# Kernel optimization log

Hardware: AMD Instinct MI355X
Metric: run time of the kernel (lower is better)

Reference implementation:

```python
import jax, jax.numpy as jnp
import numpy as np
from jax import lax

B, N, C, NP, NS, H, L = 2, 16384, 256, 2048, 32, 4, 2
DFF = 2 * C
RADIUS = 1.0
EPS = 1e-5


def setup_inputs() -> dict:
    key = jax.random.key(0)
    ks = jax.random.split(key, 12)
    s = 0.02
    f32 = jnp.float32
    return {
        "xyz": jax.random.normal(ks[0], (B, N, 3), f32),
        "features": jax.random.normal(ks[1], (B, C, N), f32),
        # positional encoding: Conv1x1(3->C/2)+BN(eval)+ReLU, Conv1x1(C/2->C)
        "pe1_w": jax.random.normal(ks[2], (C // 2, 3), f32) * s,
        "pe1_b": jnp.zeros((C // 2,), f32),
        "bn_g": jnp.ones((C // 2,), f32),
        "bn_b": jnp.zeros((C // 2,), f32),
        "bn_m": jnp.zeros((C // 2,), f32),
        "bn_v": jnp.ones((C // 2,), f32),
        "pe2_w": jax.random.normal(ks[3], (C, C // 2), f32) * s,
        "pe2_b": jnp.zeros((C,), f32),
        # L pre-norm transformer encoder layers (stacked on leading dim)
        "ipw": jax.random.normal(ks[4], (L, 3 * C, C), f32) * s,
        "ipb": jnp.zeros((L, 3 * C), f32),
        "opw": jax.random.normal(ks[5], (L, C, C), f32) * s,
        "opb": jnp.zeros((L, C), f32),
        "ln1s": jnp.ones((L, C), f32), "ln1b": jnp.zeros((L, C), f32),
        "ln2s": jnp.ones((L, C), f32), "ln2b": jnp.zeros((L, C), f32),
        "fc1w": jax.random.normal(ks[6], (L, DFF, C), f32) * s,
        "fc1b": jnp.zeros((L, DFF), f32),
        "fc2w": jax.random.normal(ks[7], (L, C, DFF), f32) * s,
        "fc2b": jnp.zeros((L, C), f32),
    }


def _fps(xyz, npoint):
    # D-FPS starting from point 0 (pointnet2 convention). xyz: [B,N,3]
    b, n, _ = xyz.shape

    def step(carry, _):
        dists, far = carry
        centroid = jnp.take_along_axis(xyz, far[:, None, None], axis=1)  # [B,1,3]
        d = jnp.sum((xyz - centroid) ** 2, -1)
        dists = jnp.minimum(dists, d)
        return (dists, jnp.argmax(dists, -1).astype(jnp.int32)), far

    init = (jnp.full((b, n), 1e10, jnp.float32), jnp.zeros((b,), jnp.int32))
    _, idx = lax.scan(step, init, None, length=npoint)
    return idx.T  # [B, npoint]


def _ball_query(xyz, new_xyz, radius, ns):
    # first <=ns points within radius, padded with the first hit. [B,NP,NS]
    n = xyz.shape[1]
    d2 = jnp.sum((new_xyz[:, :, None, :] - xyz[:, None, :, :]) ** 2, -1)  # [B,NP,N]
    scores = jnp.where(d2 < radius * radius, jnp.arange(n, dtype=jnp.int32), n)
    svals = jnp.sort(scores, axis=-1)[..., :ns]
    order = jnp.argsort(scores, axis=-1)[..., :ns].astype(jnp.int32)
    valid = svals < n
    return jnp.where(valid, order, order[..., :1])


def _ln(x, s, b):
    m = jnp.mean(x, -1, keepdims=True)
    v = jnp.var(x, -1, keepdims=True)
    return (x - m) * lax.rsqrt(v + EPS) * s + b


def _mha(x, w, bias, ow, ob):
    # x: [S, Bn, D] (seq-first, like nn.MultiheadAttention)
    S, Bn, D = x.shape
    hd = D // H
    qkv = x @ w.T + bias
    q, k, v = jnp.split(qkv, 3, -1)
    rs = lambda t: t.reshape(S, Bn, H, hd).transpose(1, 2, 0, 3)  # [Bn,H,S,hd]
    q, k, v = rs(q), rs(k), rs(v)
    att = jax.nn.softmax(jnp.einsum('bhqd,bhkd->bhqk', q, k) * (1.0 / np.sqrt(hd)), -1)
    o = jnp.einsum('bhqk,bhkd->bhqd', att, v).transpose(2, 0, 1, 3).reshape(S, Bn, D)
    return o @ ow.T + ob


def reference(xyz, features, pe1_w, pe1_b, bn_g, bn_b, bn_m, bn_v, pe2_w, pe2_b,
              ipw, ipb, opw, opb, ln1s, ln1b, ln2s, ln2b, fc1w, fc1b, fc2w, fc2b):
    # --- sample + group ---
    fps_idx = _fps(lax.stop_gradient(xyz), NP)                       # [B,NP]
    new_xyz = jnp.take_along_axis(xyz, fps_idx[:, :, None], axis=1)  # [B,NP,3]
    idx = _ball_query(lax.stop_gradient(xyz), lax.stop_gradient(new_xyz), RADIUS, NS)
    g_xyz = jax.vmap(lambda p, i: p[i])(xyz, idx) - new_xyz[:, :, None, :]  # [B,NP,NS,3]
    g_xyz = g_xyz.transpose(0, 3, 1, 2)                              # [B,3,NP,NS]
    g_feat = jax.vmap(lambda f, i: f[:, i])(features, idx)           # [B,C,NP,NS]
    # --- positional encoding (conv1x1 + BN(eval) + ReLU, conv1x1) ---
    h = jnp.einsum('oc,bcps->bops', pe1_w, g_xyz) + pe1_b[None, :, None, None]
    h = (h - bn_m[None, :, None, None]) * lax.rsqrt(bn_v + EPS)[None, :, None, None]
    h = jax.nn.relu(h * bn_g[None, :, None, None] + bn_b[None, :, None, None])
    pe = jnp.einsum('oc,bcps->bops', pe2_w, h) + pe2_b[None, :, None, None]
    x = g_feat + pe                                                  # [B,C,NP,NS]
    # --- local transformer over each neighborhood (seq len = NS) ---
    x = x.transpose(0, 2, 1, 3).reshape(B * NP, C, NS).transpose(2, 0, 1)  # [NS,B*NP,C]
    for l in range(L):
        x = _ln(x, ln1s[l], ln1b[l])
        x = x + _mha(x, ipw[l], ipb[l], opw[l], opb[l])
        x = _ln(x, ln2s[l], ln2b[l])
        x = x + jax.nn.relu(x @ fc1w[l].T + fc1b[l]) @ fc2w[l].T + fc2b[l]
    tf = x.transpose(1, 2, 0).reshape(B, NP, C, NS).transpose(0, 2, 1, 3)  # [B,C,NP,NS]
    Lf = NP * NS

    def scat(feat_b, tf_b, idx_b):
        idx_f = idx_b.reshape(-1)          # [Lf]
        ff = tf_b.reshape(C, -1)           # [C,Lf]
        pos = jnp.arange(Lf, dtype=jnp.int32)
        first = jax.ops.segment_min(pos, idx_f, num_segments=N)  # [N], maxint if absent
        valid = first < Lf
        safe = jnp.where(valid, first, 0)
        return jnp.where(valid[None, :], ff[:, safe], feat_b)    # [C,N]

    out = jax.vmap(scat)(features, tf, idx)  # [B,C,N]
    return out.transpose(0, 2, 1)            # [B,N,C]
```

## Files before the change

kernel.cpp:

```cpp
#include <hip/hip_runtime.h>

#define NB 2
#define NN 16384
#define NC 256
#define NPp 2048
#define NSs 32
#define NH 4
#define HDh 64
#define NL 2
#define NDFF 512
#define LFv (NPp*NSs)
#define LNEPS 1e-5f
#define NBLK 256
#define NTHR 512

typedef short s16x8 __attribute__((ext_vector_type(8)));
typedef float f32x4 __attribute__((ext_vector_type(4)));
typedef float f32x2 __attribute__((ext_vector_type(2)));
typedef unsigned short u16;
typedef unsigned long long u64;

struct CtlBlock { int prog[2]; int ctr1; int ctr2; int bar; };

__device__ __forceinline__ u16 f2bf(float f){
  unsigned u = __float_as_uint(f);
  u += 0x7fffu + ((u>>16)&1u);
  return (u16)(u>>16);
}

__device__ __forceinline__ f32x4 mfma16(s16x8 a, s16x8 b, f32x4 c){
  return __builtin_amdgcn_mfma_f32_16x16x32_bf16(a, b, c, 0, 0, 0);
}

__device__ __forceinline__ f32x2 pk_add(f32x2 a, f32x2 b){
  f32x2 d; asm("v_pk_add_f32 %0, %1, %2" : "=v"(d) : "v"(a), "v"(b)); return d;
}
__device__ __forceinline__ f32x2 pk_mul(f32x2 a, f32x2 b){
  f32x2 d; asm("v_pk_mul_f32 %0, %1, %2" : "=v"(d) : "v"(a), "v"(b)); return d;
}

#define DPP_FMAX(v, ctrl) do { \
  int _iv = __float_as_int(v); \
  int _sh = __builtin_amdgcn_update_dpp(_iv, _iv, (ctrl), 0xF, 0xF, false); \
  (v) = fmaxf((v), __int_as_float(_sh)); \
} while(0)

#define DPP_IMIN(v, ctrl) do { \
  int _sh = __builtin_amdgcn_update_dpp((v), (v), (ctrl), 0xF, 0xF, false); \
  (v) = (_sh < (v)) ? _sh : (v); \
} while(0)

struct SMem {
  u64  masks[256];
  u64  wvkey[2][8];
  float wvc[2][8][4];
  int  idxbuf[8];
  float xs[32][260];
  u16  xn[32][264];
  u16  qb[32][776];
  u16  pb[NH][32][40];
  int  idx_sh[32];
  float gx_sh[32][3];
  int  misc[16];
  int  win[32];
};

__global__ void k_prep(const float* __restrict__ ipw, const float* __restrict__ opw,
                       const float* __restrict__ fc1w, const float* __restrict__ fc2w,
                       const float* __restrict__ pe2w,
                       const float* __restrict__ bng, const float* __restrict__ bnb,
                       const float* __restrict__ bnm, const float* __restrict__ bnv,
                       u16* ipwb, u16* opwb, u16* fc1wb, u16* fc2wb, u16* pe2wb,
                       float* bnsc, float* bnsh, int* first, CtlBlock* ctl){
  const int i0 = blockIdx.x*blockDim.x + threadIdx.x;
  const int stride = gridDim.x*blockDim.x;
  for (int i=i0; i<NL*768*NC; i+=stride) ipwb[i] = f2bf(ipw[i]);
  for (int i=i0; i<NL*NC*NC; i+=stride)  opwb[i] = f2bf(opw[i]);
  for (int i=i0; i<NL*NDFF*NC; i+=stride) fc1wb[i] = f2bf(fc1w[i]);
  for (int i=i0; i<NL*NC*NDFF; i+=stride) fc2wb[i] = f2bf(fc2w[i]);
  for (int i=i0; i<NC*128; i+=stride)    pe2wb[i] = f2bf(pe2w[i]);
  for (int i=i0; i<NB*NN; i+=stride)     first[i] = LFv;
  for (int i=i0; i<128; i+=stride){
    float sc = bng[i]*rsqrtf(bnv[i]+LNEPS);
    bnsc[i] = sc; bnsh[i] = bnb[i] - bnm[i]*sc;
  }
  if (i0 == 0){
    ctl->prog[0] = -1; ctl->prog[1] = -1;
    ctl->ctr1 = 0; ctl->ctr2 = 0; ctl->bar = 0;
  }
}

__global__ __launch_bounds__(256) void k_featT(const float* __restrict__ feat,
                                               float* __restrict__ featT){
  __shared__ float T[32][33];
  const int b = blockIdx.y;
  const int n0 = blockIdx.x*32;
  const int t = threadIdx.x;
  const int tn = t & 31, tc = t >> 5;
  for (int cb=0; cb<NC; cb+=32){
    #pragma unroll
    for (int i=0;i<32;i+=8)
      T[tc+i][tn] = feat[((size_t)b*NC + cb+tc+i)*NN + n0+tn];
    __syncthreads();
    #pragma unroll
    for (int i=0;i<32;i+=8)
      featT[((size_t)b*NN + n0+tc+i)*NC + cb+tn] = T[tn][tc+i];
    __syncthreads();
  }
}

#define SELC(S) case S: scx = px2[(S)>>1][(S)&1]; scy = py2[(S)>>1][(S)&1]; scz = pz2[(S)>>1][(S)&1]; break;

__device__ void fps_run(int b, const float* __restrict__ xyz, int* __restrict__ fps_idx,
                        CtlBlock* ctl, SMem& sm){
#pragma clang fp contract(off)
  const int t = threadIdx.x;
  const int lane = t & 63, wid = t >> 6;
  const float* xb = xyz + (size_t)b*NN*3;
  f32x2 px2[16], py2[16], pz2[16], dd2[16];
  #pragma unroll
  for (int m=0;m<16;m++){
    int i0 = t + (2*m)*NTHR, i1 = t + (2*m+1)*NTHR;
    px2[m] = f32x2{xb[i0*3],   xb[i1*3]};
    py2[m] = f32x2{xb[i0*3+1], xb[i1*3+1]};
    pz2[m] = f32x2{xb[i0*3+2], xb[i1*3+2]};
    dd2[m] = f32x2{1e10f, 1e10f};
  }
  float ncx, ncy, ncz;
  {
    float wx = xb[0], wy = xb[1], wz = xb[2];
    ncx=-wx; ncy=-wy; ncz=-wz;
    if (t==0){
      fps_idx[b*NPp] = 0;
      __hip_atomic_store(&ctl->prog[b], 0, __ATOMIC_RELEASE, __HIP_MEMORY_SCOPE_AGENT);
    }
  }
  __syncthreads();
  for (int step=1; step<NPp; ++step){
    const f32x2 ncx2={ncx,ncx}, ncy2={ncy,ncy}, ncz2={ncz,ncz};
    #pragma unroll
    for (int m=0;m<16;m++){
      f32x2 dx = pk_add(px2[m], ncx2);
      f32x2 dy = pk_add(py2[m], ncy2);
      f32x2 dz = pk_add(pz2[m], ncz2);
      f32x2 s  = pk_add(pk_add(pk_mul(dx,dx), pk_mul(dy,dy)), pk_mul(dz,dz));
      f32x2 d  = dd2[m];
      d.x = fminf(d.x, s.x);
      d.y = fminf(d.y, s.y);
      dd2[m] = d;
    }
    float h8[8];
    #pragma unroll
    for (int q=0;q<8;q++)
      h8[q] = fmaxf(fmaxf(dd2[2*q].x, dd2[2*q].y), fmaxf(dd2[2*q+1].x, dd2[2*q+1].y));
    float M = fmaxf(fmaxf(fmaxf(h8[0],h8[1]),fmaxf(h8[2],h8[3])),
                    fmaxf(fmaxf(h8[4],h8[5]),fmaxf(h8[6],h8[7])));
    DPP_FMAX(M, 0x111); DPP_FMAX(M, 0x112); DPP_FMAX(M, 0x114); DPP_FMAX(M, 0x118);
    DPP_FMAX(M, 0x142); DPP_FMAX(M, 0x143);
    const int Mi = __builtin_amdgcn_readlane(__float_as_int(M), 63);
    const float Ms = __int_as_float(Mi);
    int li = 0x7fffffff;
    #pragma unroll
    for (int m=15;m>=0;m--){
      if (dd2[m].y == Ms) li = t + (2*m+1)*NTHR;
      if (dd2[m].x == Ms) li = t + (2*m)*NTHR;
    }
    DPP_IMIN(li, 0x111); DPP_IMIN(li, 0x112); DPP_IMIN(li, 0x114); DPP_IMIN(li, 0x118);
    DPP_IMIN(li, 0x142); DPP_IMIN(li, 0x143);
    const int liw = __builtin_amdgcn_readlane(li, 63);
    const int sb = step & 1;
    if (lane==0)
      sm.wvkey[sb][wid] = ((u64)(unsigned)Mi << 32) | (unsigned)(0x7fffffff - liw);
    {
      const int slot = liw >> 9;
      float scx=0.f, scy=0.f, scz=0.f;
      switch(slot){
        SELC(0) SELC(1) SELC(2) SELC(3) SELC(4) SELC(5) SELC(6) SELC(7)
        SELC(8) SELC(9) SELC(10) SELC(11) SELC(12) SELC(13) SELC(14) SELC(15)
        SELC(16) SELC(17) SELC(18) SELC(19) SELC(20) SELC(21) SELC(22) SELC(23)
        SELC(24) SELC(25) SELC(26) SELC(27) SELC(28) SELC(29) SELC(30) SELC(31)
        default: break;
      }
      if (t == (liw & (NTHR-1))){
        sm.wvc[sb][wid][0]=scx; sm.wvc[sb][wid][1]=scy; sm.wvc[sb][wid][2]=scz;
      }
    }
    __syncthreads();
    u64 bk = sm.wvkey[sb][0];
    float bx=sm.wvc[sb][0][0], by=sm.wvc[sb][0][1], bz=sm.wvc[sb][0][2];
    #pragma unroll
    for (int w=1;w<8;w++){
      u64 k2 = sm.wvkey[sb][w];
      if (k2 > bk){ bk=k2; bx=sm.wvc[sb][w][0]; by=sm.wvc[sb][w][1]; bz=sm.wvc[sb][w][2]; }
    }
    ncx=-bx; ncy=-by; ncz=-bz;
    if (t==0){
      int widx = 0x7fffffff - (int)(unsigned)(bk & 0xffffffffu);
      sm.idxbuf[step & 7] = widx;
      if ((step & 7) == 7){
        int s0 = step - 7;
        #pragma unroll
        for (int j=0;j<8;j++){
          int s = s0 + j;
          if (s > 0) fps_idx[b*NPp + s] = sm.idxbuf[s & 7];
        }
        __hip_atomic_store(&ctl->prog[b], step, __ATOMIC_RELEASE, __HIP_MEMORY_SCOPE_AGENT);
      }
    }
  }
}

__device__ void seq_ballq(const float* __restrict__ xb, float cx, float cy, float cz,
                          SMem& sm, int t, int lane, int wid){
#pragma clang fp contract(off)
  for (int it=0; it<32; ++it){
    int cid = wid*32 + it;
    int i = cid*64 + lane;
    float dx=xb[i*3]-cx, dy=xb[i*3+1]-cy, dz=xb[i*3+2]-cz;
    float d2=(dx*dx+dy*dy)+dz*dz;
    u64 m = __ballot(d2 < 1.0f);
    if (lane==0) sm.masks[cid] = m;
  }
  __syncthreads();
  if (wid==0){
    u64 mk[4]; int cnt=0;
    #pragma unroll
    for (int j=0;j<4;j++){ mk[j]=sm.masks[lane*4+j]; cnt += __popcll(mk[j]); }
    int inc = cnt;
    #pragma unroll
    for (int ofs=1; ofs<64; ofs<<=1){
      int v = __shfl_up(inc, ofs);
      if (lane >= ofs) inc += v;
    }
    int r = inc - cnt;
    int tot = __shfl(inc, 63);
    #pragma unroll
    for (int j=0;j<4;j++){
      u64 msk = mk[j];
      int base = (lane*4+j)*64;
      while (msk && r < NSs){
        int bpos = __ffsll(msk)-1;
        sm.idx_sh[r] = base + bpos;
        msk &= msk-1;
        ++r;
      }
      if (r >= NSs) break;
    }
    int cc = tot < NSs ? tot : NSs;
    int pv = (tot > 0) ? sm.idx_sh[0] : 0;
    if (lane < NSs && lane >= cc) sm.idx_sh[lane] = pv;
  }
  __syncthreads();
}

__device__ __forceinline__ void ln_block512(SMem& sm, const float* __restrict__ s_,
                                            const float* __restrict__ b_, int t){
  const int s = t >> 4, j = t & 15;
  float v[16];
  float sum = 0.f;
  #pragma unroll
  for (int k=0;k<16;k++){ v[k]=sm.xs[s][j*16+k]; sum += v[k]; }
  #pragma unroll
  for (int m=1;m<16;m<<=1) sum += __shfl_xor(sum, m);
  const float mean = sum * (1.f/256.f);
  float vs = 0.f;
  #pragma unroll
  for (int k=0;k<16;k++){ float d=v[k]-mean; vs += d*d; }
  #pragma unroll
  for (int m=1;m<16;m<<=1) vs += __shfl_xor(vs, m);
  const float rstd = rsqrtf(vs*(1.f/256.f) + LNEPS);
  #pragma unroll
  for (int k=0;k<16;k++){
    int c = j*16+k;
    float y = (v[k]-mean)*rstd*s_[c] + b_[c];
    sm.xs[s][c] = y;
    sm.xn[s][c] = f2bf(y);
  }
}

__device__ void seq_pe_tf(SMem& sm, int b, float ccx, float ccy, float ccz,
    const float* __restrict__ xyz, const float* __restrict__ features,
    const float* __restrict__ featT, int useT,
    const float* __restrict__ pe1w, const float* __restrict__ pe1b,
    const float* __restrict__ bnsc, const float* __restrict__ bnsh,
    const u16* __restrict__ pe2wb, const float* __restrict__ pe2b,
    const u16* __restrict__ ipwb, const float* __restrict__ ipb,
    const u16* __restrict__ opwb, const float* __restrict__ opb,
    const float* __restrict__ ln1s, const float* __restrict__ ln1b,
    const float* __restrict__ ln2s, const float* __restrict__ ln2b,
    const u16* __restrict__ fc1wb, const float* __restrict__ fc1b,
    const u16* __restrict__ fc2wb, const float* __restrict__ fc2b){
  const int t = threadIdx.x, lane = t & 63, wid = t >> 6;
  const int c15 = lane & 15, g4 = lane >> 4;

  if (t < 96){
    int s = t/3, d = t%3;
    float cd = (d==0) ? ccx : ((d==1) ? ccy : ccz);
    sm.gx_sh[s][d] = xyz[((size_t)b*NN + sm.idx_sh[s])*3 + d] - cd;
  }
  if (useT){
    for (int e=t; e<32*NC; e+=NTHR){
      int s=e>>8, c=e&255;
      sm.xs[s][c] = featT[((size_t)b*NN + sm.idx_sh[s])*NC + c];
    }
  } else {
    for (int e=t; e<32*NC; e+=NTHR){
      int s=e>>8, c=e&255;
      sm.xs[s][c] = features[((size_t)b*NC + c)*NN + sm.idx_sh[s]];
    }
  }
  __syncthreads();
  for (int i=t; i<32*128; i+=NTHR){
    int s = i >> 7, o = i & 127;
    float h = pe1w[o*3]*sm.gx_sh[s][0] + pe1w[o*3+1]*sm.gx_sh[s][1] + pe1w[o*3+2]*sm.gx_sh[s][2] + pe1b[o];
    h = h*bnsc[o] + bnsh[o];
    sm.xn[s][o] = f2bf(h > 0.f ? h : 0.f);
  }
  __syncthreads();
  for (int tt=wid; tt<32; tt+=8){
    int m0 = (tt & 1)*16, n0 = (tt >> 1)*16;
    f32x4 acc = {0.f,0.f,0.f,0.f};
    #pragma unroll
    for (int kk=0; kk<4; kk++){
      s16x8 a = *(const s16x8*)&sm.xn[m0+c15][kk*32 + g4*8];
      s16x8 bb = *(const s16x8*)&pe2wb[(size_t)(n0+c15)*128 + kk*32 + g4*8];
      acc = mfma16(a, bb, acc);
    }
    int col = n0 + c15;
    float bias = pe2b[col];
    #pragma unroll
    for (int r=0;r<4;r++) sm.xs[m0 + g4*4 + r][col] += acc[r] + bias;
  }
  __syncthreads();

  for (int l=0; l<NL; ++l){
    ln_block512(sm, ln1s + l*NC, ln1b + l*NC, t);
    __syncthreads();
    const u16* Wq = ipwb + (size_t)l*768*NC;
    const float* bq = ipb + l*768;
    for (int tt=wid; tt<96; tt+=8){
      int m0 = (tt & 1)*16, n0 = (tt >> 1)*16;
      f32x4 acc = {0.f,0.f,0.f,0.f};
      #pragma unroll
      for (int kk=0;kk<8;kk++){
        s16x8 a = *(const s16x8*)&sm.xn[m0+c15][kk*32 + g4*8];
        s16x8 bb = *(const s16x8*)&Wq[(size_t)(n0+c15)*NC + kk*32 + g4*8];
        acc = mfma16(a, bb, acc);
      }
      int col = n0 + c15;
      float bias = bq[col];
      #pragma unroll
      for (int r=0;r<4;r++) sm.qb[m0 + g4*4 + r][col] = f2bf(acc[r] + bias);
    }
    __syncthreads();
    {
      const int h = wid & 3;
      const int mt = wid >> 2;
      f32x4 lac[2];
      #pragma unroll
      for (int nt=0;nt<2;nt++){
        f32x4 acc = {0.f,0.f,0.f,0.f};
        #pragma unroll
        for (int kk=0;kk<2;kk++){
          s16x8 a = *(const s16x8*)&sm.qb[mt*16+c15][h*HDh + kk*32 + g4*8];
          s16x8 bb = *(const s16x8*)&sm.qb[nt*16+c15][256 + h*HDh + kk*32 + g4*8];
          acc = mfma16(a, bb, acc);
        }
        lac[nt] = acc;
      }
      #pragma unroll
      for (int r=0;r<4;r++){
        float v0 = lac[0][r]*0.125f, v1 = lac[1][r]*0.125f;
        float mx = fmaxf(v0, v1);
        #pragma unroll
        for (int m=1;m<16;m<<=1) mx = fmaxf(mx, __shfl_xor(mx, m));
        float e0 = expf(v0-mx), e1 = expf(v1-mx);
        float smm = e0 + e1;
        #pragma unroll
        for (int m=1;m<16;m<<=1) smm += __shfl_xor(smm, m);
        float inv = 1.f/smm;
        int row = mt*16 + g4*4 + r;
        sm.pb[h][row][c15]    = f2bf(e0*inv);
        sm.pb[h][row][16+c15] = f2bf(e1*inv);
      }
      f32x4 oac[4];
      #pragma unroll
      for (int nt=0;nt<4;nt++){
        s16x8 bb;
        #pragma unroll
        for (int e=0;e<8;e++) bb[e] = (short)sm.qb[g4*8+e][512 + h*HDh + nt*16 + c15];
        f32x4 acc = {0.f,0.f,0.f,0.f};
        s16x8 a = *(const s16x8*)&sm.pb[h][mt*16+c15][g4*8];
        oac[nt] = mfma16(a, bb, acc);
      }
      __syncthreads();
      #pragma unroll
      for (int nt=0;nt<4;nt++)
        #pragma unroll
        for (int r=0;r<4;r++)
          sm.xn[mt*16 + g4*4 + r][h*HDh + nt*16 + c15] = f2bf(oac[nt][r]);
    }
    __syncthreads();
    const u16* Wo = opwb + (size_t)l*NC*NC;
    const float* bo = opb + l*NC;
    for (int tt=wid; tt<32; tt+=8){
      int m0 = (tt & 1)*16, n0 = (tt >> 1)*16;
      f32x4 acc = {0.f,0.f,0.f,0.f};
      #pragma unroll
      for (int kk=0;kk<8;kk++){
        s16x8 a = *(const s16x8*)&sm.xn[m0+c15][kk*32 + g4*8];
        s16x8 bb = *(const s16x8*)&Wo[(size_t)(n0+c15)*NC + kk*32 + g4*8];
        acc = mfma16(a, bb, acc);
      }
      int col = n0 + c15;
      float bias = bo[col];
      #pragma unroll
      for (int r=0;r<4;r++) sm.xs[m0 + g4*4 + r][col] += acc[r] + bias;
    }
    __syncthreads();
    ln_block512(sm, ln2s + l*NC, ln2b + l*NC, t);
    __syncthreads();
    const u16* W1 = fc1wb + (size_t)l*NDFF*NC;
    for (int tt=wid; tt<64; tt+=8){
      int m0 = (tt & 1)*16, n0 = (tt >> 1)*16;
      f32x4 acc = {0.f,0.f,0.f,0.f};
      #pragma unroll
      for (int kk=0;kk<8;kk++){
        s16x8 a = *(const s16x8*)&sm.xn[m0+c15][kk*32 + g4*8];
        s16x8 bb = *(const s16x8*)&W1[(size_t)(n0+c15)*NC + kk*32 + g4*8];
        acc = mfma16(a, bb, acc);
      }
      int col = n0 + c15;
      float bias = fc1b[l*NDFF + col];
      #pragma unroll
      for (int r=0;r<4;r++){
        float v = acc[r] + bias;
        sm.qb[m0 + g4*4 + r][col] = f2bf(v > 0.f ? v : 0.f);
      }
    }
    __syncthreads();
    const u16* W2 = fc2wb + (size_t)l*NC*NDFF;
    for (int tt=wid; tt<32; tt+=8){
      int m0 = (tt & 1)*16, n0 = (tt >> 1)*16;
      f32x4 acc = {0.f,0.f,0.f,0.f};
      #pragma unroll
      for (int kk=0;kk<16;kk++){
        s16x8 a = *(const s16x8*)&sm.qb[m0+c15][kk*32 + g4*8];
        s16x8 bb = *(const s16x8*)&W2[(size_t)(n0+c15)*NDFF + kk*32 + g4*8];
        acc = mfma16(a, bb, acc);
      }
      int col = n0 + c15;
      float bias = fc2b[l*NC + col];
      #pragma unroll
      for (int r=0;r<4;r++) sm.xs[m0 + g4*4 + r][col] += acc[r] + bias;
    }
    __syncthreads();
  }
}

__global__ __launch_bounds__(NTHR,1) void k_mega(
    const float* __restrict__ xyz, const float* __restrict__ features,
    const float* __restrict__ featT, int useT, u16* __restrict__ tfb, int spec,
    int* __restrict__ fps_idx, int* __restrict__ first, CtlBlock* ctl,
    const float* __restrict__ pe1w, const float* __restrict__ pe1b,
    const float* __restrict__ bnsc, const float* __restrict__ bnsh,
    const u16* __restrict__ pe2wb, const float* __restrict__ pe2b,
    const u16* __restrict__ ipwb, const float* __restrict__ ipb,
    const u16* __restrict__ opwb, const float* __restrict__ opb,
    const float* __restrict__ ln1s, const float* __restrict__ ln1b,
    const float* __restrict__ ln2s, const float* __restrict__ ln2b,
    const u16* __restrict__ fc1wb, const float* __restrict__ fc1b,
    const u16* __restrict__ fc2wb, const float* __restrict__ fc2b,
    float* __restrict__ out){
  __shared__ SMem sm;
  const int t = threadIdx.x, lane = t & 63, wid = t >> 6;

  if (blockIdx.x < NB){
    fps_run(blockIdx.x, xyz, fps_idx, ctl, sm);
  } else {
    for (;;){
      if (t==0) sm.misc[1] = atomicAdd(&ctl->ctr1, 1);
      __syncthreads();
      int p = sm.misc[1];
      if (p >= NB*NPp) break;
      int b = p >> 11, pp = p & (NPp-1);
      if (t==0){
        while (__hip_atomic_load(&ctl->prog[b], __ATOMIC_RELAXED, __HIP_MEMORY_SCOPE_AGENT) < pp)
          __builtin_amdgcn_s_sleep(2);
        __builtin_amdgcn_fence(__ATOMIC_ACQUIRE, "agent");
        sm.misc[4] = fps_idx[p];
      }
      __syncthreads();
      int ci = sm.misc[4];
      float cx = xyz[((size_t)b*NN + ci)*3];
      float cy = xyz[((size_t)b*NN + ci)*3+1];
      float cz = xyz[((size_t)b*NN + ci)*3+2];
      seq_ballq(xyz + (size_t)b*NN*3, cx, cy, cz, sm, t, lane, wid);
      if (t < NSs) atomicMin(&first[b*NN + sm.idx_sh[t]], pp*NSs + t);
      if (spec){
        seq_pe_tf(sm, b, cx, cy, cz, xyz, features, featT, useT,
                  pe1w, pe1b, bnsc, bnsh, pe2wb, pe2b, ipwb, ipb, opwb, opb,
                  ln1s, ln1b, ln2s, ln2b, fc1wb, fc1b, fc2wb, fc2b);
        for (int e=t; e<NSs*NC; e+=NTHR)
          tfb[(size_t)p*NSs*NC + e] = f2bf(sm.xs[e>>8][e&255]);
      }
      __syncthreads();
    }
  }
  if (spec) return;

  __syncthreads();
  if (t==0){
    __builtin_amdgcn_fence(__ATOMIC_RELEASE, "agent");
    __hip_atomic_fetch_add(&ctl->bar, 1, __ATOMIC_RELAXED, __HIP_MEMORY_SCOPE_AGENT);
    while (__hip_atomic_load(&ctl->bar, __ATOMIC_RELAXED, __HIP_MEMORY_SCOPE_AGENT) < NBLK)
      __builtin_amdgcn_s_sleep(8);
    __builtin_amdgcn_fence(__ATOMIC_ACQUIRE, "agent");
  }
  __syncthreads();
  for (;;){
    if (t==0) sm.misc[1] = atomicAdd(&ctl->ctr2, 1);
    __syncthreads();
    int p = sm.misc[1];
    if (p >= NB*NPp) break;
    int b = p >> 11, pp = p & (NPp-1);
    int ci = fps_idx[p];
    float cx = xyz[((size_t)b*NN + ci)*3];
    float cy = xyz[((size_t)b*NN + ci)*3+1];
    float cz = xyz[((size_t)b*NN + ci)*3+2];
    seq_ballq(xyz + (size_t)b*NN*3, cx, cy, cz, sm, t, lane, wid);
    if (t==0) sm.misc[2] = 0;
    __syncthreads();
    if (t < NSs){
      int pos = pp*NSs + t;
      int f = __hip_atomic_load(&first[b*NN + sm.idx_sh[t]], __ATOMIC_RELAXED, __HIP_MEMORY_SCOPE_AGENT);
      int w = (f == pos) ? 1 : 0;
      sm.win[t] = w;
      if (w) atomicOr(&sm.misc[2], 1);
    }
    __syncthreads();
    if (!sm.misc[2]) continue;
    seq_pe_tf(sm, b, cx, cy, cz, xyz, features, featT, useT,
              pe1w, pe1b, bnsc, bnsh, pe2wb, pe2b, ipwb, ipb, opwb, opb,
              ln1s, ln1b, ln2s, ln2b, fc1wb, fc1b, fc2wb, fc2b);
    for (int e=t; e<NSs*NC; e+=NTHR){
      int s = e >> 8, c = e & 255;
      if (sm.win[s]) out[((size_t)b*NN + sm.idx_sh[s])*NC + c] = sm.xs[s][c];
    }
    __syncthreads();
  }
}

__global__ __launch_bounds__(256) void k_commit(const u16* __restrict__ tfb,
                                                const int* __restrict__ first,
                                                const float* __restrict__ featT,
                                                const float* __restrict__ feat,
                                                int useT, float* __restrict__ out){
  const int t = threadIdx.x;
  const int row0 = blockIdx.x*16;
  for (int r=0;r<16;++r){
    int row = row0 + r;
    int b = row >> 14;
    int f = first[row];
    float v;
    if (f != LFv){
      unsigned u = tfb[((size_t)b*NPp*NSs + f)*NC + t];
      v = __int_as_float((int)(u << 16));
    } else if (useT){
      v = featT[(size_t)row*NC + t];
    } else {
      int n = row & (NN-1);
      v = feat[((size_t)b*NC + t)*NN + n];
    }
    out[(size_t)row*NC + t] = v;
  }
}

__global__ __launch_bounds__(256) void k_outfill_T(const float* __restrict__ featT,
                                                   const int* __restrict__ first,
                                                   float* __restrict__ out){
  const int t = threadIdx.x;
  for (int rr=0; rr<8; ++rr){
    int row = blockIdx.x*8 + rr;
    if (first[row] == LFv)
      out[(size_t)row*NC + t] = featT[(size_t)row*NC + t];
  }
}

__global__ __launch_bounds__(256) void k_outfill_noT(const float* __restrict__ feat,
                                                     const int* __restrict__ first,
                                                     float* __restrict__ out){
  __shared__ float T[32][33];
  const int b = blockIdx.y;
  const int n0 = blockIdx.x*32;
  const int t = threadIdx.x;
  const int tn = t & 31, tc = t >> 5;
  for (int cb=0; cb<NC; cb+=32){
    #pragma unroll
    for (int i=0;i<32;i+=8)
      T[tc+i][tn] = feat[((size_t)b*NC + cb+tc+i)*NN + n0+tn];
    __syncthreads();
    #pragma unroll
    for (int i=0;i<32;i+=8){
      int n = n0 + tc + i;
      if (first[b*NN+n] == LFv)
        out[((size_t)b*NN + n)*NC + cb+tn] = T[tn][tc+i];
    }
    __syncthreads();
  }
}

extern "C" void kernel_launch(void* const* d_in, const int* in_sizes, int n_in,
                              void* d_out, int out_size, void* d_ws, size_t ws_size,
                              hipStream_t stream){
  const float* xyz   = (const float*)d_in[0];
  const float* feat  = (const float*)d_in[1];
  const float* pe1w  = (const float*)d_in[2];
  const float* pe1b  = (const float*)d_in[3];
  const float* bng   = (const float*)d_in[4];
  const float* bnb   = (const float*)d_in[5];
  const float* bnm   = (const float*)d_in[6];
  const float* bnv   = (const float*)d_in[7];
  const float* pe2w  = (const float*)d_in[8];
  const float* pe2b  = (const float*)d_in[9];
  const float* ipw   = (const float*)d_in[10];
  const float* ipb   = (const float*)d_in[11];
  const float* opw   = (const float*)d_in[12];
  const float* opb   = (const float*)d_in[13];
  const float* ln1s  = (const float*)d_in[14];
  const float* ln1b  = (const float*)d_in[15];
  const float* ln2s  = (const float*)d_in[16];
  const float* ln2b  = (const float*)d_in[17];
  const float* fc1w  = (const float*)d_in[18];
  const float* fc1b  = (const float*)d_in[19];
  const float* fc2w  = (const float*)d_in[20];
  const float* fc2b  = (const float*)d_in[21];
  float* out = (float*)d_out;

  char* ws = (char*)d_ws;
  size_t off = 0;
  auto alloc = [&](size_t bytes)->void*{
    void* p = ws + off;
    off = (off + bytes + 255) & ~(size_t)255;
    return p;
  };
  int*   fps_idx = (int*)  alloc((size_t)NB*NPp*4);
  int*   first   = (int*)  alloc((size_t)NB*NN*4);
  CtlBlock* ctl  = (CtlBlock*)alloc(sizeof(CtlBlock));
  float* bnsc    = (float*)alloc(128*4);
  float* bnsh    = (float*)alloc(128*4);
  u16*   ipwb    = (u16*)  alloc((size_t)NL*768*NC*2);
  u16*   opwb    = (u16*)  alloc((size_t)NL*NC*NC*2);
  u16*   fc1wb   = (u16*)  alloc((size_t)NL*NDFF*NC*2);
  u16*   fc2wb   = (u16*)  alloc((size_t)NL*NC*NDFF*2);
  u16*   pe2wb   = (u16*)  alloc((size_t)NC*128*2);
  int useT = (off + (size_t)NB*NN*NC*4 <= ws_size) ? 1 : 0;
  float* featT = (float*)(useT ? alloc((size_t)NB*NN*NC*4) : (void*)ws);
  int spec = (off + (size_t)NB*NPp*NSs*NC*2 <= ws_size) ? 1 : 0;
  u16* tfb = (u16*)(spec ? alloc((size_t)NB*NPp*NSs*NC*2) : (void*)ws);

  k_prep<<<512, 256, 0, stream>>>(ipw, opw, fc1w, fc2w, pe2w, bng, bnb, bnm, bnv,
                                  ipwb, opwb, fc1wb, fc2wb, pe2wb, bnsc, bnsh, first, ctl);
  if (useT)
    k_featT<<<dim3(NN/32, NB), 256, 0, stream>>>(feat, featT);

  const float* featT_c = featT;
  void* kargs[] = {
    (void*)&xyz, (void*)&feat, (void*)&featT_c, (void*)&useT, (void*)&tfb, (void*)&spec,
    (void*)&fps_idx, (void*)&first, (void*)&ctl,
    (void*)&pe1w, (void*)&pe1b, (void*)&bnsc, (void*)&bnsh,
    (void*)&pe2wb, (void*)&pe2b, (void*)&ipwb, (void*)&ipb,
    (void*)&opwb, (void*)&opb, (void*)&ln1s, (void*)&ln1b,
    (void*)&ln2s, (void*)&ln2b, (void*)&fc1wb, (void*)&fc1b,
    (void*)&fc2wb, (void*)&fc2b, (void*)&out };
  hipLaunchCooperativeKernel((void*)k_mega, dim3(NBLK), dim3(NTHR), kargs, 0, stream);

  if (spec){
    k_commit<<<(NB*NN)/16, 256, 0, stream>>>(tfb, first, featT, feat, useT, out);
  } else if (useT){
    k_outfill_T<<<(NB*NN)/8, 256, 0, stream>>>(featT, first, out);
  } else {
    k_outfill_noT<<<dim3(NN/32, NB), 256, 0, stream>>>(feat, first, out);
  }
  (void)in_sizes; (void)n_in; (void)out_size;
}
```

Baseline: 5.295 ms.

## Double block size to 1024 threads and publish FPS centroid coordinates directly

Raises the persistent kernel's block size from 512 to 1024 threads (16 waves), so each FPS block holds fewer points per thread and the transformer GEMM loops spread over more waves. The FPS argmax index search now uses per-wave ballots and a shuffle reduction instead of DPP min chains and a serial scan. Consumers read centroid xyz published as packed 64-bit words rather than an index followed by a dependent xyz gather. Acquire/release ordering is replaced with relaxed atomics plus explicit waitcnt, and progress is published one step later. This adds register pressure, idles half the waves in attention, and relies on hand-written memory ordering for correctness.

```diff
diff --git a/kernel.cpp b/kernel.cpp
--- a/kernel.cpp
+++ b/kernel.cpp
@@ -12,7 +12,8 @@
 #define LFv (NPp*NSs)
 #define LNEPS 1e-5f
 #define NBLK 256
-#define NTHR 512
+#define NTHR 1024
+#define NW 16
 
 typedef short s16x8 __attribute__((ext_vector_type(8)));
 typedef float f32x4 __attribute__((ext_vector_type(4)));
@@ -45,16 +46,11 @@
   (v) = fmaxf((v), __int_as_float(_sh)); \
 } while(0)
 
-#define DPP_IMIN(v, ctrl) do { \
-  int _sh = __builtin_amdgcn_update_dpp((v), (v), (ctrl), 0xF, 0xF, false); \
-  (v) = (_sh < (v)) ? _sh : (v); \
-} while(0)
-
 struct SMem {
   u64  masks[256];
-  u64  wvkey[2][8];
-  float wvc[2][8][4];
-  int  idxbuf[8];
+  u64  wvkey[2][NW];
+  float wvc[2][NW][4];
+  float cxbuf[8][4];
   float xs[32][260];
   u16  xn[32][264];
   u16  qb[32][776];
@@ -111,15 +107,16 @@
 
 #define SELC(S) case S: scx = px2[(S)>>1][(S)&1]; scy = py2[(S)>>1][(S)&1]; scz = pz2[(S)>>1][(S)&1]; break;
 
-__device__ void fps_run(int b, const float* __restrict__ xyz, int* __restrict__ fps_idx,
+__device__ void fps_run(int b, const float* __restrict__ xyz, u64* __restrict__ cx2,
                         CtlBlock* ctl, SMem& sm){
 #pragma clang fp contract(off)
   const int t = threadIdx.x;
   const int lane = t & 63, wid = t >> 6;
+  const int wbase = wid*64;
   const float* xb = xyz + (size_t)b*NN*3;
-  f32x2 px2[16], py2[16], pz2[16], dd2[16];
+  f32x2 px2[8], py2[8], pz2[8], dd2[8];
   #pragma unroll
-  for (int m=0;m<16;m++){
+  for (int m=0;m<8;m++){
     int i0 = t + (2*m)*NTHR, i1 = t + (2*m+1)*NTHR;
     px2[m] = f32x2{xb[i0*3],   xb[i1*3]};
     py2[m] = f32x2{xb[i0*3+1], xb[i1*3+1]};
@@ -131,15 +128,21 @@
     float wx = xb[0], wy = xb[1], wz = xb[2];
     ncx=-wx; ncy=-wy; ncz=-wz;
     if (t==0){
-      fps_idx[b*NPp] = 0;
-      __hip_atomic_store(&ctl->prog[b], 0, __ATOMIC_RELEASE, __HIP_MEMORY_SCOPE_AGENT);
+      sm.cxbuf[0][0]=wx; sm.cxbuf[0][1]=wy; sm.cxbuf[0][2]=wz;
+      u64 lo = ((u64)__float_as_uint(wy) << 32) | __float_as_uint(wx);
+      u64 hi = (u64)__float_as_uint(wz);
+      __hip_atomic_store(&cx2[(size_t)(b*NPp)*2],   lo, __ATOMIC_RELAXED, __HIP_MEMORY_SCOPE_AGENT);
+      __hip_atomic_store(&cx2[(size_t)(b*NPp)*2+1], hi, __ATOMIC_RELAXED, __HIP_MEMORY_SCOPE_AGENT);
+      asm volatile("s_waitcnt vmcnt(0)" ::: "memory");
+      __hip_atomic_store(&ctl->prog[b], 0, __ATOMIC_RELAXED, __HIP_MEMORY_SCOPE_AGENT);
     }
   }
   __syncthreads();
   for (int step=1; step<NPp; ++step){
     const f32x2 ncx2={ncx,ncx}, ncy2={ncy,ncy}, ncz2={ncz,ncz};
-    #pragma unroll
-    for (int m=0;m<16;m++){
+    float bestv = -1.f;
+    #pragma unroll
+    for (int m=0;m<8;m++){
       f32x2 dx = pk_add(px2[m], ncx2);
       f32x2 dy = pk_add(py2[m], ncy2);
       f32x2 dz = pk_add(pz2[m], ncz2);
@@ -148,73 +151,82 @@
       d.x = fminf(d.x, s.x);
       d.y = fminf(d.y, s.y);
       dd2[m] = d;
-    }
-    float h8[8];
-    #pragma unroll
-    for (int q=0;q<8;q++)
-      h8[q] = fmaxf(fmaxf(dd2[2*q].x, dd2[2*q].y), fmaxf(dd2[2*q+1].x, dd2[2*q+1].y));
-    float M = fmaxf(fmaxf(fmaxf(h8[0],h8[1]),fmaxf(h8[2],h8[3])),
-                    fmaxf(fmaxf(h8[4],h8[5]),fmaxf(h8[6],h8[7])));
+      bestv = fmaxf(fmaxf(bestv, d.x), d.y);
+    }
+    float M = bestv;
     DPP_FMAX(M, 0x111); DPP_FMAX(M, 0x112); DPP_FMAX(M, 0x114); DPP_FMAX(M, 0x118);
     DPP_FMAX(M, 0x142); DPP_FMAX(M, 0x143);
     const int Mi = __builtin_amdgcn_readlane(__float_as_int(M), 63);
     const float Ms = __int_as_float(Mi);
-    int li = 0x7fffffff;
-    #pragma unroll
-    for (int m=15;m>=0;m--){
-      if (dd2[m].y == Ms) li = t + (2*m+1)*NTHR;
-      if (dd2[m].x == Ms) li = t + (2*m)*NTHR;
-    }
-    DPP_IMIN(li, 0x111); DPP_IMIN(li, 0x112); DPP_IMIN(li, 0x114); DPP_IMIN(li, 0x118);
-    DPP_IMIN(li, 0x142); DPP_IMIN(li, 0x143);
-    const int liw = __builtin_amdgcn_readlane(li, 63);
+    u64 bs[16];
+    #pragma unroll
+    for (int m=0;m<8;m++){
+      bs[2*m]   = __ballot(dd2[m].x == Ms);
+      bs[2*m+1] = __ballot(dd2[m].y == Ms);
+    }
+    int li = 0;
+    #pragma unroll
+    for (int s=15;s>=0;s--)
+      if (bs[s]) li = wbase + s*NTHR + (__ffsll(bs[s])-1);
     const int sb = step & 1;
     if (lane==0)
-      sm.wvkey[sb][wid] = ((u64)(unsigned)Mi << 32) | (unsigned)(0x7fffffff - liw);
+      sm.wvkey[sb][wid] = ((u64)(unsigned)Mi << 32) | (unsigned)(0x7fffffff - li);
     {
-      const int slot = liw >> 9;
+      const int slot = li >> 10;
       float scx=0.f, scy=0.f, scz=0.f;
       switch(slot){
         SELC(0) SELC(1) SELC(2) SELC(3) SELC(4) SELC(5) SELC(6) SELC(7)
         SELC(8) SELC(9) SELC(10) SELC(11) SELC(12) SELC(13) SELC(14) SELC(15)
-        SELC(16) SELC(17) SELC(18) SELC(19) SELC(20) SELC(21) SELC(22) SELC(23)
-        SELC(24) SELC(25) SELC(26) SELC(27) SELC(28) SELC(29) SELC(30) SELC(31)
         default: break;
       }
-      if (t == (liw & (NTHR-1))){
+      if (t == (li & (NTHR-1))){
         sm.wvc[sb][wid][0]=scx; sm.wvc[sb][wid][1]=scy; sm.wvc[sb][wid][2]=scz;
       }
     }
     __syncthreads();
-    u64 bk = sm.wvkey[sb][0];
-    float bx=sm.wvc[sb][0][0], by=sm.wvc[sb][0][1], bz=sm.wvc[sb][0][2];
-    #pragma unroll
-    for (int w=1;w<8;w++){
-      u64 k2 = sm.wvkey[sb][w];
-      if (k2 > bk){ bk=k2; bx=sm.wvc[sb][w][0]; by=sm.wvc[sb][w][1]; bz=sm.wvc[sb][w][2]; }
-    }
+    u64 v = sm.wvkey[sb][lane & 15];
+    #pragma unroll
+    for (int m=1;m<16;m<<=1){
+      u64 o = __shfl_xor(v, m);
+      if (o > v) v = o;
+    }
+    const int widx = 0x7fffffff - (int)(unsigned)(v & 0xffffffffull);
+    const int wv = (widx & (NTHR-1)) >> 6;
+    const float bx = sm.wvc[sb][wv][0];
+    const float by = sm.wvc[sb][wv][1];
+    const float bz = sm.wvc[sb][wv][2];
     ncx=-bx; ncy=-by; ncz=-bz;
     if (t==0){
-      int widx = 0x7fffffff - (int)(unsigned)(bk & 0xffffffffu);
-      sm.idxbuf[step & 7] = widx;
+      sm.cxbuf[step & 7][0]=bx; sm.cxbuf[step & 7][1]=by; sm.cxbuf[step & 7][2]=bz;
       if ((step & 7) == 7){
         int s0 = step - 7;
         #pragma unroll
         for (int j=0;j<8;j++){
-          int s = s0 + j;
-          if (s > 0) fps_idx[b*NPp + s] = sm.idxbuf[s & 7];
+          float fx=sm.cxbuf[j][0], fy=sm.cxbuf[j][1], fz=sm.cxbuf[j][2];
+          u64 lo = ((u64)__float_as_uint(fy) << 32) | __float_as_uint(fx);
+          u64 hi = (u64)__float_as_uint(fz);
+          size_t pb2 = (size_t)(b*NPp + s0 + j)*2;
+          __hip_atomic_store(&cx2[pb2],   lo, __ATOMIC_RELAXED, __HIP_MEMORY_SCOPE_AGENT);
+          __hip_atomic_store(&cx2[pb2+1], hi, __ATOMIC_RELAXED, __HIP_MEMORY_SCOPE_AGENT);
         }
-        __hip_atomic_store(&ctl->prog[b], step, __ATOMIC_RELEASE, __HIP_MEMORY_SCOPE_AGENT);
-      }
-    }
+      }
+      if ((step & 7) == 0){
+        asm volatile("s_waitcnt vmcnt(0)" ::: "memory");
+        __hip_atomic_store(&ctl->prog[b], step-1, __ATOMIC_RELAXED, __HIP_MEMORY_SCOPE_AGENT);
+      }
+    }
+  }
+  if (t==0){
+    asm volatile("s_waitcnt vmcnt(0)" ::: "memory");
+    __hip_atomic_store(&ctl->prog[b], NPp, __ATOMIC_RELAXED, __HIP_MEMORY_SCOPE_AGENT);
   }
 }
 
 __device__ void seq_ballq(const float* __restrict__ xb, float cx, float cy, float cz,
                           SMem& sm, int t, int lane, int wid){
 #pragma clang fp contract(off)
-  for (int it=0; it<32; ++it){
-    int cid = wid*32 + it;
+  for (int it=0; it<16; ++it){
+    int cid = wid*16 + it;
     int i = cid*64 + lane;
     float dx=xb[i*3]-cx, dy=xb[i*3+1]-cy, dz=xb[i*3+2]-cz;
     float d2=(dx*dx+dy*dy)+dz*dz;
@@ -253,25 +265,25 @@
   __syncthreads();
 }
 
-__device__ __forceinline__ void ln_block512(SMem& sm, const float* __restrict__ s_,
-                                            const float* __restrict__ b_, int t){
-  const int s = t >> 4, j = t & 15;
-  float v[16];
+__device__ __forceinline__ void ln_block1024(SMem& sm, const float* __restrict__ s_,
+                                             const float* __restrict__ b_, int t){
+  const int s = t >> 5, j = t & 31;
+  float v[8];
   float sum = 0.f;
   #pragma unroll
-  for (int k=0;k<16;k++){ v[k]=sm.xs[s][j*16+k]; sum += v[k]; }
+  for (int k=0;k<8;k++){ v[k]=sm.xs[s][j*8+k]; sum += v[k]; }
   #pragma unroll
-  for (int m=1;m<16;m<<=1) sum += __shfl_xor(sum, m);
+  for (int m=1;m<32;m<<=1) sum += __shfl_xor(sum, m);
   const float mean = sum * (1.f/256.f);
   float vs = 0.f;
   #pragma unroll
-  for (int k=0;k<16;k++){ float d=v[k]-mean; vs += d*d; }
+  for (int k=0;k<8;k++){ float d=v[k]-mean; vs += d*d; }
   #pragma unroll
-  for (int m=1;m<16;m<<=1) vs += __shfl_xor(vs, m);
+  for (int m=1;m<32;m<<=1) vs += __shfl_xor(vs, m);
   const float rstd = rsqrtf(vs*(1.f/256.f) + LNEPS);
   #pragma unroll
-  for (int k=0;k<16;k++){
-    int c = j*16+k;
+  for (int k=0;k<8;k++){
+    int c = j*8+k;
     float y = (v[k]-mean)*rstd*s_[c] + b_[c];
     sm.xs[s][c] = y;
     sm.xn[s][c] = f2bf(y);
@@ -317,7 +329,7 @@
     sm.xn[s][o] = f2bf(h > 0.f ? h : 0.f);
   }
   __syncthreads();
-  for (int tt=wid; tt<32; tt+=8){
+  for (int tt=wid; tt<32; tt+=NW){
     int m0 = (tt & 1)*16, n0 = (tt >> 1)*16;
     f32x4 acc = {0.f,0.f,0.f,0.f};
     #pragma unroll
@@ -334,11 +346,11 @@
   __syncthreads();
 
   for (int l=0; l<NL; ++l){
-    ln_block512(sm, ln1s + l*NC, ln1b + l*NC, t);
+    ln_block1024(sm, ln1s + l*NC, ln1b + l*NC, t);
     __syncthreads();
     const u16* Wq = ipwb + (size_t)l*768*NC;
     const float* bq = ipb + l*768;
-    for (int tt=wid; tt<96; tt+=8){
+    for (int tt=wid; tt<96; tt+=NW){
       int m0 = (tt & 1)*16, n0 = (tt >> 1)*16;
       f32x4 acc = {0.f,0.f,0.f,0.f};
       #pragma unroll
@@ -355,55 +367,59 @@
     __syncthreads();
     {
       const int h = wid & 3;
-      const int mt = wid >> 2;
-      f32x4 lac[2];
-      #pragma unroll
-      for (int nt=0;nt<2;nt++){
-        f32x4 acc = {0.f,0.f,0.f,0.f};
+      const int mt = (wid >> 2) & 1;
+      f32x4 oac[4];
+      if (wid < 8){
+        f32x4 lac[2];
         #pragma unroll
-        for (int kk=0;kk<2;kk++){
-          s16x8 a = *(const s16x8*)&sm.qb[mt*16+c15][h*HDh + kk*32 + g4*8];
-          s16x8 bb = *(const s16x8*)&sm.qb[nt*16+c15][256 + h*HDh + kk*32 + g4*8];
-          acc = mfma16(a, bb, acc);
+        for (int nt=0;nt<2;nt++){
+          f32x4 acc = {0.f,0.f,0.f,0.f};
+          #pragma unroll
+          for (int kk=0;kk<2;kk++){
+            s16x8 a = *(const s16x8*)&sm.qb[mt*16+c15][h*HDh + kk*32 + g4*8];
+            s16x8 bb = *(const s16x8*)&sm.qb[nt*16+c15][256 + h*HDh + kk*32 + g4*8];
+            acc = mfma16(a, bb, acc);
+          }
+          lac[nt] = acc;
         }
-        lac[nt] = acc;
-      }
-      #pragma unroll
-      for (int r=0;r<4;r++){
-        float v0 = lac[0][r]*0.125f, v1 = lac[1][r]*0.125f;
-        float mx = fmaxf(v0, v1);
         #pragma unroll
-        for (int m=1;m<16;m<<=1) mx = fmaxf(mx, __shfl_xor(mx, m));
-        float e0 = expf(v0-mx), e1 = expf(v1-mx);
-        float smm = e0 + e1;
+        for (int r=0;r<4;r++){
+          float v0 = lac[0][r]*0.125f, v1 = lac[1][r]*0.125f;
+          float mx = fmaxf(v0, v1);
+          #pragma unroll
+          for (int m=1;m<16;m<<=1) mx = fmaxf(mx, __shfl_xor(mx, m));
+          float e0 = expf(v0-mx), e1 = expf(v1-mx);
+          float smm = e0 + e1;
+          #pragma unroll
+          for (int m=1;m<16;m<<=1) smm += __shfl_xor(smm, m);
+          float inv = 1.f/smm;
+          int row = mt*16 + g4*4 + r;
+          sm.pb[h][row][c15]    = f2bf(e0*inv);
+          sm.pb[h][row][16+c15] = f2bf(e1*inv);
+        }
         #pragma unroll
-        for (int m=1;m<16;m<<=1) smm += __shfl_xor(smm, m);
-        float inv = 1.f/smm;
-        int row = mt*16 + g4*4 + r;
-        sm.pb[h][row][c15]    = f2bf(e0*inv);
-        sm.pb[h][row][16+c15] = f2bf(e1*inv);
-      }
-      f32x4 oac[4];
-      #pragma unroll
-      for (int nt=0;nt<4;nt++){
-        s16x8 bb;
+        for (int nt=0;nt<4;nt++){
+          s16x8 bb;
+          #pragma unroll
+          for (int e=0;e<8;e++) bb[e] = (short)sm.qb[g4*8+e][512 + h*HDh + nt*16 + c15];
+          f32x4 acc = {0.f,0.f,0.f,0.f};
+          s16x8 a = *(const s16x8*)&sm.pb[h][mt*16+c15][g4*8];
+          oac[nt] = mfma16(a, bb, acc);
+        }
+      }
+      __syncthreads();
+      if (wid < 8){
         #pragma unroll
-        for (int e=0;e<8;e++) bb[e] = (short)sm.qb[g4*8+e][512 + h*HDh + nt*16 + c15];
-        f32x4 acc = {0.f,0.f,0.f,0.f};
-        s16x8 a = *(const s16x8*)&sm.pb[h][mt*16+c15][g4*8];
-        oac[nt] = mfma16(a, bb, acc);
-      }
-      __syncthreads();
-      #pragma unroll
-      for (int nt=0;nt<4;nt++)
-        #pragma unroll
-        for (int r=0;r<4;r++)
-          sm.xn[mt*16 + g4*4 + r][h*HDh + nt*16 + c15] = f2bf(oac[nt][r]);
+        for (int nt=0;nt<4;nt++)
+          #pragma unroll
+          for (int r=0;r<4;r++)
+            sm.xn[mt*16 + g4*4 + r][h*HDh + nt*16 + c15] = f2bf(oac[nt][r]);
+      }
     }
     __syncthreads();
     const u16* Wo = opwb + (size_t)l*NC*NC;
     const float* bo = opb + l*NC;
-    for (int tt=wid; tt<32; tt+=8){
+    for (int tt=wid; tt<32; tt+=NW){
       int m0 = (tt & 1)*16, n0 = (tt >> 1)*16;
       f32x4 acc = {0.f,0.f,0.f,0.f};
       #pragma unroll
@@ -418,10 +434,10 @@
       for (int r=0;r<4;r++) sm.xs[m0 + g4*4 + r][col] += acc[r] + bias;
     }
     __syncthreads();
-    ln_block512(sm, ln2s + l*NC, ln2b + l*NC, t);
+    ln_block1024(sm, ln2s + l*NC, ln2b + l*NC, t);
     __syncthreads();
     const u16* W1 = fc1wb + (size_t)l*NDFF*NC;
-    for (int tt=wid; tt<64; tt+=8){
+    for (int tt=wid; tt<64; tt+=NW){
       int m0 = (tt & 1)*16, n0 = (tt >> 1)*16;
       f32x4 acc = {0.f,0.f,0.f,0.f};
       #pragma unroll
@@ -440,7 +456,7 @@
     }
     __syncthreads();
     const u16* W2 = fc2wb + (size_t)l*NC*NDFF;
-    for (int tt=wid; tt<32; tt+=8){
+    for (int tt=wid; tt<32; tt+=NW){
       int m0 = (tt & 1)*16, n0 = (tt >> 1)*16;
       f32x4 acc = {0.f,0.f,0.f,0.f};
       #pragma unroll
@@ -458,10 +474,10 @@
   }
 }
 
-__global__ __launch_bounds__(NTHR,1) void k_mega(
+__global__ __launch_bounds__(NTHR) void k_mega(
     const float* __restrict__ xyz, const float* __restrict__ features,
     const float* __restrict__ featT, int useT, u16* __restrict__ tfb, int spec,
-    int* __restrict__ fps_idx, int* __restrict__ first, CtlBlock* ctl,
+    u64* __restrict__ cx2, int* __restrict__ first, CtlBlock* ctl,
     const float* __restrict__ pe1w, const float* __restrict__ pe1b,
     const float* __restrict__ bnsc, const float* __restrict__ bnsh,
     const u16* __restrict__ pe2wb, const float* __restrict__ pe2b,
@@ -476,7 +492,7 @@
   const int t = threadIdx.x, lane = t & 63, wid = t >> 6;
 
   if (blockIdx.x < NB){
-    fps_run(blockIdx.x, xyz, fps_idx, ctl, sm);
+    fps_run(blockIdx.x, xyz, cx2, ctl, sm);
   } else {
     for (;;){
       if (t==0) sm.misc[1] = atomicAdd(&ctl->ctr1, 1);
@@ -487,14 +503,17 @@
       if (t==0){
         while (__hip_atomic_load(&ctl->prog[b], __ATOMIC_RELAXED, __HIP_MEMORY_SCOPE_AGENT) < pp)
           __builtin_amdgcn_s_sleep(2);
-        __builtin_amdgcn_fence(__ATOMIC_ACQUIRE, "agent");
-        sm.misc[4] = fps_idx[p];
+        asm volatile("" ::: "memory");
+        u64 lo = __hip_atomic_load(&cx2[(size_t)p*2],   __ATOMIC_RELAXED, __HIP_MEMORY_SCOPE_AGENT);
+        u64 hi = __hip_atomic_load(&cx2[(size_t)p*2+1], __ATOMIC_RELAXED, __HIP_MEMORY_SCOPE_AGENT);
+        sm.misc[4] = (int)(unsigned)(lo & 0xffffffffull);
+        sm.misc[5] = (int)(unsigned)(lo >> 32);
+        sm.misc[6] = (int)(unsigned)(hi & 0xffffffffull);
       }
       __syncthreads();
-      int ci = sm.misc[4];
-      float cx = xyz[((size_t)b*NN + ci)*3];
-      float cy = xyz[((size_t)b*NN + ci)*3+1];
-      float cz = xyz[((size_t)b*NN + ci)*3+2];
+      float cx = __int_as_float(sm.misc[4]);
+      float cy = __int_as_float(sm.misc[5]);
+      float cz = __int_as_float(sm.misc[6]);
       seq_ballq(xyz + (size_t)b*NN*3, cx, cy, cz, sm, t, lane, wid);
       if (t < NSs) atomicMin(&first[b*NN + sm.idx_sh[t]], pp*NSs + t);
       if (spec){
@@ -524,10 +543,10 @@
     int p = sm.misc[1];
     if (p >= NB*NPp) break;
     int b = p >> 11, pp = p & (NPp-1);
-    int ci = fps_idx[p];
-    float cx = xyz[((size_t)b*NN + ci)*3];
-    float cy = xyz[((size_t)b*NN + ci)*3+1];
-    float cz = xyz[((size_t)b*NN + ci)*3+2];
+    u64 lo = cx2[(size_t)p*2], hi = cx2[(size_t)p*2+1];
+    float cx = __int_as_float((int)(unsigned)(lo & 0xffffffffull));
+    float cy = __int_as_float((int)(unsigned)(lo >> 32));
+    float cz = __int_as_float((int)(unsigned)(hi & 0xffffffffull));
     seq_ballq(xyz + (size_t)b*NN*3, cx, cy, cz, sm, t, lane, wid);
     if (t==0) sm.misc[2] = 0;
     __syncthreads();
@@ -644,7 +663,7 @@
     off = (off + bytes + 255) & ~(size_t)255;
     return p;
   };
-  int*   fps_idx = (int*)  alloc((size_t)NB*NPp*4);
+  u64*   cx2     = (u64*)  alloc((size_t)NB*NPp*2*8);
   int*   first   = (int*)  alloc((size_t)NB*NN*4);
   CtlBlock* ctl  = (CtlBlock*)alloc(sizeof(CtlBlock));
   float* bnsc    = (float*)alloc(128*4);
@@ -667,7 +686,7 @@
   const float* featT_c = featT;
   void* kargs[] = {
     (void*)&xyz, (void*)&feat, (void*)&featT_c, (void*)&useT, (void*)&tfb, (void*)&spec,
-    (void*)&fps_idx, (void*)&first, (void*)&ctl,
+    (void*)&cx2, (void*)&first, (void*)&ctl,
     (void*)&pe1w, (void*)&pe1b, (void*)&bnsc, (void*)&bnsh,
     (void*)&pe2wb, (void*)&pe2b, (void*)&ipwb, (void*)&ipb,
     (void*)&opwb, (void*)&opb, (void*)&ln1s, (void*)&ln1b,
```

Result: slower. 5.736 ms (+8.3%).
